# Performance work log

Measured on AMD Instinct MI355X. Metric: run time of the kernel, lower is better.

Reference implementation:

```python
import jax, jax.numpy as jnp
import numpy as np

N_NODES = 50000
N_EDGES = 800000
DIM_IN = 128
DIM_H = 128
DIM_OUT = 10
N_GRAPHS = 256


def _glorot(key, shape):
    lim = float(np.sqrt(6.0 / (shape[0] + shape[1])))
    return jax.random.uniform(key, shape, jnp.float32, -lim, lim)


def setup_inputs() -> dict:
    key = jax.random.key(0)
    ks = jax.random.split(key, 8)
    x = jax.random.normal(ks[0], (N_NODES, DIM_IN), jnp.float32)
    edge_index = jax.random.randint(ks[1], (2, N_EDGES), 0, N_NODES, dtype=jnp.int64)
    batch = jnp.sort(jax.random.randint(ks[2], (N_NODES,), 0, N_GRAPHS, dtype=jnp.int64))
    return {
        'x': x,
        'edge_index': edge_index,
        'batch': batch,
        'W1': _glorot(ks[3], (DIM_IN, DIM_H)),
        'b1': jnp.zeros((DIM_H,), jnp.float32),
        'W2': _glorot(ks[4], (DIM_H, DIM_H)),
        'b2': jnp.zeros((DIM_H,), jnp.float32),
        'Wl1': _glorot(ks[5], (2 * DIM_H, 2 * DIM_H)),
        'bl1': jnp.zeros((2 * DIM_H,), jnp.float32),
        'Wl2': _glorot(ks[6], (2 * DIM_H, DIM_OUT)),
        'bl2': jnp.zeros((DIM_OUT,), jnp.float32),
    }


def _gcn_conv(h, W, b, src, dst, norm, n):
    # x @ W, gather source rows, scale by symmetric norm, scatter-add to dest
    m = (h @ W)[src] * norm[:, None]          # [E+N, dim_h]
    return jax.ops.segment_sum(m, dst, num_segments=n) + b


def reference(x, edge_index, batch, W1, b1, W2, b2, Wl1, bl1, Wl2, bl2):
    n = x.shape[0]
    loops = jnp.arange(n, dtype=edge_index.dtype)
    src = jnp.concatenate([edge_index[0], loops])  # add self-loops (PyG GCNConv default)
    dst = jnp.concatenate([edge_index[1], loops])
    deg = jax.ops.segment_sum(jnp.ones_like(dst, x.dtype), dst, num_segments=n)
    dinv = jnp.where(deg > 0, jax.lax.rsqrt(jnp.maximum(deg, 1.0)), 0.0)
    norm = dinv[src] * dinv[dst]
    # eval mode: dropout is identity
    h1 = _gcn_conv(x, W1, b1, src, dst, norm, n)
    h2 = _gcn_conv(h1, W2, b2, src, dst, norm, n)
    g1 = jax.ops.segment_sum(h1, batch, num_segments=N_GRAPHS)  # global_add_pool
    g2 = jax.ops.segment_sum(h2, batch, num_segments=N_GRAPHS)
    g = jnp.concatenate([g1, g2], axis=1)  # [N_GRAPHS, 2*dim_h]
    h = jax.nn.relu(g @ Wl1 + bl1)
    h = h @ Wl2 + bl2
    return (h, jax.nn.log_softmax(h, axis=1))
```

## Files before the change

### kernel.cpp

```cpp
#include <hip/hip_runtime.h>
#include <hip/hip_bf16.h>
#include <math.h>


#define DIMH 128
#define EBCAP 8192
#define SCAT_CHUNK 2048

typedef __attribute__((ext_vector_type(8))) short s16x8;
typedef __attribute__((ext_vector_type(4))) float f32x4;

__device__ inline ushort f2b(float f) {
    uint u = __float_as_uint(f);
    return (ushort)((u + 0x7fffu + ((u >> 16) & 1u)) >> 16);
}
__device__ inline uint pack2(float lo, float hi) {
    return (uint)f2b(lo) | ((uint)f2b(hi) << 16);
}
__device__ inline float blo(uint u) { return __uint_as_float(u << 16); }
__device__ inline float bhi(uint u) { return __uint_as_float(u & 0xffff0000u); }

__global__ __launch_bounds__(256) void k_front(const int* __restrict__ src,
                                               const int* __restrict__ dst,
                                               int* __restrict__ bcnt,
                                               uint* __restrict__ ebuf, int E, int scnb,
                                               const float* __restrict__ x,
                                               ushort* __restrict__ Xb, int n8, int cvnb,
                                               const float* __restrict__ W1,
                                               const float* __restrict__ W2,
                                               ushort* __restrict__ WT1,
                                               ushort* __restrict__ WT2) {
    __shared__ int h[4][256];
    __shared__ int wb[4][256];
    int blk = blockIdx.x;
    int t = threadIdx.x;
    if (blk < scnb) {
        int wave = t >> 6;
        h[0][t] = 0; h[1][t] = 0; h[2][t] = 0; h[3][t] = 0;
        __syncthreads();
        int e0 = blk * SCAT_CHUNK;
        int e1 = e0 + SCAT_CHUNK; if (e1 > E) e1 = E;
        for (int e = e0 + t; e < e1; e += 256)
            atomicAdd(&h[wave][dst[e] >> 8], 1);
        __syncthreads();
        {
            int h0 = h[0][t], h1 = h[1][t], h2 = h[2][t], h3 = h[3][t];
            int tot = h0 + h1 + h2 + h3;
            int gb = tot ? atomicAdd(&bcnt[t], tot) : 0;
            wb[0][t] = gb;
            wb[1][t] = gb + h0;
            wb[2][t] = gb + h0 + h1;
            wb[3][t] = gb + h0 + h1 + h2;
            h[0][t] = 0; h[1][t] = 0; h[2][t] = 0; h[3][t] = 0;
        }
        __syncthreads();
        for (int e = e0 + t; e < e1; e += 256) {
            int d = dst[e];
            int bk = d >> 8;
            int rank = wb[wave][bk] + atomicAdd(&h[wave][bk], 1);
            if (rank < EBCAP)
                ebuf[(size_t)bk * EBCAP + rank] = ((uint)(d & 255) << 24) | (uint)src[e];
        }
    } else if (blk < scnb + cvnb) {
        int i = (blk - scnb) * 256 + t;
        if (i < n8) {
            const float4* in4 = (const float4*)x;
            float4 a = in4[2 * i], b = in4[2 * i + 1];
            uint4 o;
            o.x = pack2(a.x, a.y); o.y = pack2(a.z, a.w);
            o.z = pack2(b.x, b.y); o.w = pack2(b.z, b.w);
            *(uint4*)(Xb + (size_t)i * 8) = o;
        }
    } else {
        int idx = (blk - scnb - cvnb) * 256 + t;
        const float* W = (idx < 16384) ? W1 : W2;
        ushort* WT = (idx < 16384) ? WT1 : WT2;
        int tt = idx & 16383;
        int k = tt >> 7, nn = tt & 127;
        WT[nn * 128 + k] = f2b(W[tt]);
    }
}

__global__ __launch_bounds__(256) void k_bcsr(const uint* __restrict__ ebuf,
                                              const int* __restrict__ bcnt,
                                              float* __restrict__ dinv,
                                              int2* __restrict__ rng,
                                              int* __restrict__ srt, int n) {
    __shared__ int cnt[256];
    __shared__ int wsum[4];
    __shared__ int stage[EBCAP];
    int b = blockIdx.x;
    int t = threadIdx.x;
    int c = bcnt[b]; if (c > EBCAP) c = EBCAP;
    size_t B = (size_t)b * EBCAP;
    cnt[t] = 0;
    __syncthreads();
    for (int i = t; i < c; i += 256)
        atomicAdd(&cnt[ebuf[B + i] >> 24], 1);
    __syncthreads();
    int v = cnt[t];
    int incl = v;
    for (int k = 1; k < 64; k <<= 1) {
        int u = __shfl_up(incl, k, 64);
        if ((t & 63) >= k) incl += u;
    }
    if ((t & 63) == 63) wsum[t >> 6] = incl;
    __syncthreads();
    int add = 0;
    for (int j = 0; j < (t >> 6); ++j) add += wsum[j];
    incl += add;
    int loc = incl - v;
    int node = b * 256 + t;
    if (node < n) {
        dinv[node] = rsqrtf((float)(v + 1));
        rng[node] = make_int2((int)B + loc, (int)B + loc + v);
    }
    cnt[t] = loc;
    __syncthreads();
    for (int i = t; i < c; i += 256) {
        uint r = ebuf[B + i];
        int p = atomicAdd(&cnt[r >> 24], 1);
        stage[p] = (int)(r & 0xffffffu);
    }
    __syncthreads();
    for (int i = t; i < c; i += 256) srt[B + i] = stage[i];
}

__device__ __forceinline__ void gemm_body(const ushort* __restrict__ Xb,
                                          const ushort* __restrict__ WT,
                                          const float* __restrict__ scale,
                                          ushort* __restrict__ P, int n,
                                          int blk, ushort* lds) {
    ushort* Xs = lds;
    ushort* Ws = lds + 64 * 128;
    const int tid = threadIdx.x;
    const int row0 = blk * 64;
    for (int ci = tid; ci < 1024; ci += 256) {
        int r = ci >> 4, c16 = ci & 15;
        uint dstB = (uint)(r * 256 + c16 * 16) ^ (uint)((r & 7) << 4);
        uint4 v = make_uint4(0u, 0u, 0u, 0u);
        if (row0 + r < n) v = *(const uint4*)(Xb + (size_t)(row0 + r) * 128 + c16 * 8);
        *(uint4*)((char*)Xs + dstB) = v;
    }
    for (int ci = tid; ci < 2048; ci += 256) {
        int r = ci >> 4, c16 = ci & 15;
        uint dstB = (uint)(r * 256 + c16 * 16) ^ (uint)((r & 7) << 4);
        *(uint4*)((char*)Ws + dstB) = *(const uint4*)(WT + (size_t)r * 128 + c16 * 8);
    }
    __syncthreads();
    const int wave = tid >> 6, lane = tid & 63;
    const int l15 = lane & 15, g = lane >> 4;
    f32x4 acc[8];
#pragma unroll
    for (int nt = 0; nt < 8; ++nt) acc[nt] = (f32x4){0.f, 0.f, 0.f, 0.f};
    const int tr = wave * 16 + l15;
    const uint aswz = (uint)((tr & 7) << 4);
#pragma unroll
    for (int kk = 0; kk < 4; ++kk) {
        uint aB = ((uint)(tr * 256 + kk * 64 + g * 16)) ^ aswz;
        s16x8 afrag = *(const s16x8*)((const char*)Xs + aB);
#pragma unroll
        for (int nt = 0; nt < 8; ++nt) {
            int wr = nt * 16 + l15;
            uint bB = ((uint)(wr * 256 + kk * 64 + g * 16)) ^ ((uint)((wr & 7) << 4));
            s16x8 bfrag = *(const s16x8*)((const char*)Ws + bB);
            acc[nt] = __builtin_amdgcn_mfma_f32_16x16x32_bf16(afrag, bfrag, acc[nt], 0, 0, 0);
        }
    }
    float sc[4];
#pragma unroll
    for (int reg = 0; reg < 4; ++reg) {
        int grow = row0 + wave * 16 + g * 4 + reg;
        sc[reg] = (grow < n) ? scale[grow] : 0.f;
    }
#pragma unroll
    for (int nt = 0; nt < 8; ++nt) {
        int gcol = nt * 16 + l15;
#pragma unroll
        for (int reg = 0; reg < 4; ++reg) {
            int grow = row0 + wave * 16 + g * 4 + reg;
            if (grow < n) P[(size_t)grow * 128 + gcol] = f2b(sc[reg] * acc[nt][reg]);
        }
    }
}

__global__ __launch_bounds__(256) void k_gemm(const ushort* __restrict__ Xb,
                                              const ushort* __restrict__ WT,
                                              const float* __restrict__ scale,
                                              ushort* __restrict__ P, int n) {
    __shared__ ushort lds[64 * 128 + 128 * 128];
    gemm_body(Xb, WT, scale, P, n, blockIdx.x, lds);
}

__device__ __forceinline__ void pool_body(const ushort* __restrict__ Hb,
                                          const int* __restrict__ batch,
                                          float* __restrict__ Gpart, int n,
                                          int blk, int* range, float* part) {
    int g = blk >> 2, q = blk & 3;
    if (threadIdx.x < 2) {
        int target = g + threadIdx.x;
        int lo = 0, hi = n;
        while (lo < hi) { int m = (lo + hi) >> 1; if (batch[m] < target) lo = m + 1; else hi = m; }
        range[threadIdx.x] = lo;
    }
    __syncthreads();
    int c = threadIdx.x & 127, h = threadIdx.x >> 7;
    int r = range[0] + q * 2 + h, r1 = range[1];
    float s0 = 0.f, s1 = 0.f;
    for (; r + 8 < r1; r += 16) {
        s0 += __uint_as_float((uint)Hb[(size_t)r       * 128 + c] << 16);
        s1 += __uint_as_float((uint)Hb[(size_t)(r + 8) * 128 + c] << 16);
    }
    for (; r < r1; r += 8) s0 += __uint_as_float((uint)Hb[(size_t)r * 128 + c] << 16);
    part[threadIdx.x] = s0 + s1;
    __syncthreads();
    if (threadIdx.x < 128)
        Gpart[(size_t)blk * 128 + threadIdx.x] = part[threadIdx.x] + part[threadIdx.x + 128];
}

__global__ __launch_bounds__(256) void k_pool(const ushort* __restrict__ Hb,
                                              const int* __restrict__ batch,
                                              float* __restrict__ Gpart, int n) {
    __shared__ int range[2];
    __shared__ float part[256];
    pool_body(Hb, batch, Gpart, n, blockIdx.x, range, part);
}

__global__ __launch_bounds__(256) void k_mid(const ushort* __restrict__ Hb,
                                             const ushort* __restrict__ WT,
                                             const float* __restrict__ scale,
                                             ushort* __restrict__ P, int n, int gemnb,
                                             const int* __restrict__ batch,
                                             float* __restrict__ Gpart) {
    __shared__ ushort lds[64 * 128 + 128 * 128];
    __shared__ int range[2];
    __shared__ float part[256];
    int blk = blockIdx.x;
    if (blk < gemnb) {
        gemm_body(Hb, WT, scale, P, n, blk, lds);
    } else {
        pool_body(Hb, batch, Gpart, n, blk - gemnb, range, part);
    }
}

__global__ __launch_bounds__(256) void k_aggregate(const ushort* __restrict__ Pb,
                                                   const int2* __restrict__ rng,
                                                   const int* __restrict__ srt,
                                                   const float* __restrict__ dinv,
                                                   const float* __restrict__ bias,
                                                   ushort* __restrict__ Hb, int n) {
    int wave = threadIdx.x >> 6;
    int lane = threadIdx.x & 63;
    int i = blockIdx.x * 4 + wave;
    if (i >= n) return;
    int q   = lane >> 4;
    int sub = lane & 15;
    const uint4* P4 = (const uint4*)Pb;
    float a0 = 0.f, a1 = 0.f, a2 = 0.f, a3 = 0.f;
    float a4 = 0.f, a5 = 0.f, a6 = 0.f, a7 = 0.f;
    if (q == 0) {
        uint4 u = P4[(size_t)i * 16 + sub];
        a0 = blo(u.x); a1 = bhi(u.x); a2 = blo(u.y); a3 = bhi(u.y);
        a4 = blo(u.z); a5 = bhi(u.z); a6 = blo(u.w); a7 = bhi(u.w);
    }
    int2 r2 = rng[i];
    int e1 = r2.y;
    int e  = r2.x + q;
    while (e + 12 < e1) {
        int s0 = srt[e], s1 = srt[e + 4], s2 = srt[e + 8], s3 = srt[e + 12];
        uint4 u0 = P4[(size_t)s0 * 16 + sub];
        uint4 u1 = P4[(size_t)s1 * 16 + sub];
        uint4 u2 = P4[(size_t)s2 * 16 + sub];
        uint4 u3 = P4[(size_t)s3 * 16 + sub];
        a0 += (blo(u0.x) + blo(u1.x)) + (blo(u2.x) + blo(u3.x));
        a1 += (bhi(u0.x) + bhi(u1.x)) + (bhi(u2.x) + bhi(u3.x));
        a2 += (blo(u0.y) + blo(u1.y)) + (blo(u2.y) + blo(u3.y));
        a3 += (bhi(u0.y) + bhi(u1.y)) + (bhi(u2.y) + bhi(u3.y));
        a4 += (blo(u0.z) + blo(u1.z)) + (blo(u2.z) + blo(u3.z));
        a5 += (bhi(u0.z) + bhi(u1.z)) + (bhi(u2.z) + bhi(u3.z));
        a6 += (blo(u0.w) + blo(u1.w)) + (blo(u2.w) + blo(u3.w));
        a7 += (bhi(u0.w) + bhi(u1.w)) + (bhi(u2.w) + bhi(u3.w));
        e += 16;
    }
    while (e < e1) {
        uint4 u = P4[(size_t)srt[e] * 16 + sub];
        a0 += blo(u.x); a1 += bhi(u.x); a2 += blo(u.y); a3 += bhi(u.y);
        a4 += blo(u.z); a5 += bhi(u.z); a6 += blo(u.w); a7 += bhi(u.w);
        e += 4;
    }
    a0 += __shfl_xor(a0, 16, 64); a0 += __shfl_xor(a0, 32, 64);
    a1 += __shfl_xor(a1, 16, 64); a1 += __shfl_xor(a1, 32, 64);
    a2 += __shfl_xor(a2, 16, 64); a2 += __shfl_xor(a2, 32, 64);
    a3 += __shfl_xor(a3, 16, 64); a3 += __shfl_xor(a3, 32, 64);
    a4 += __shfl_xor(a4, 16, 64); a4 += __shfl_xor(a4, 32, 64);
    a5 += __shfl_xor(a5, 16, 64); a5 += __shfl_xor(a5, 32, 64);
    a6 += __shfl_xor(a6, 16, 64); a6 += __shfl_xor(a6, 32, 64);
    a7 += __shfl_xor(a7, 16, 64); a7 += __shfl_xor(a7, 32, 64);
    if (q == 0) {
        float di = dinv[i];
        int c = sub * 8;
        float4 b0 = *(const float4*)(bias + c);
        float4 b1 = *(const float4*)(bias + c + 4);
        uint4 o;
        o.x = pack2(fmaf(di, a0, b0.x), fmaf(di, a1, b0.y));
        o.y = pack2(fmaf(di, a2, b0.z), fmaf(di, a3, b0.w));
        o.z = pack2(fmaf(di, a4, b1.x), fmaf(di, a5, b1.y));
        o.w = pack2(fmaf(di, a6, b1.z), fmaf(di, a7, b1.w));
        *(uint4*)(Hb + (size_t)i * 128 + c) = o;
    }
}

__global__ __launch_bounds__(256) void k_mlp(const float* __restrict__ Gp1,
                                             const float* __restrict__ Gp2,
                                             const float* __restrict__ Wl1,
                                             const float* __restrict__ bl1,
                                             const float* __restrict__ Wl2,
                                             const float* __restrict__ bl2,
                                             float* __restrict__ out) {
    __shared__ float gs[256];
    __shared__ float zs[256];
    __shared__ float l[10];
    int g = blockIdx.x, j = threadIdx.x;
    {
        const float* Gp = (j < 128) ? Gp1 : Gp2;
        const float* p = Gp + (size_t)g * 512 + (j & 127);
        gs[j] = (p[0] + p[128]) + (p[256] + p[384]);
    }
    __syncthreads();
    float acc = bl1[j];
    for (int k = 0; k < 256; ++k) acc = fmaf(gs[k], Wl1[k * 256 + j], acc);
    zs[j] = fmaxf(acc, 0.f);
    __syncthreads();
    if (j < 10) {
        float a = bl2[j];
        for (int k = 0; k < 256; ++k) a = fmaf(zs[k], Wl2[k * 10 + j], a);
        l[j] = a;
    }
    __syncthreads();
    if (j < 10) {
        float m = l[0];
        for (int i = 1; i < 10; ++i) m = fmaxf(m, l[i]);
        float s = 0.f;
        for (int i = 0; i < 10; ++i) s += expf(l[i] - m);
        float lse = m + logf(s);
        out[g * 10 + j] = l[j];
        out[2560 + g * 10 + j] = l[j] - lse;
    }
}

static inline size_t alignup(size_t v) { return (v + 255) & ~(size_t)255; }

extern "C" void kernel_launch(void* const* d_in, const int* in_sizes, int n_in,
                              void* d_out, int out_size, void* d_ws, size_t ws_size,
                              hipStream_t stream) {
    const float* x    = (const float*)d_in[0];
    const int*   edge = (const int*)d_in[1];
    const int*   batch= (const int*)d_in[2];
    const float* W1   = (const float*)d_in[3];
    const float* b1   = (const float*)d_in[4];
    const float* W2   = (const float*)d_in[5];
    const float* b2   = (const float*)d_in[6];
    const float* Wl1  = (const float*)d_in[7];
    const float* bl1  = (const float*)d_in[8];
    const float* Wl2  = (const float*)d_in[9];
    const float* bl2  = (const float*)d_in[10];

    const int N = in_sizes[2];
    const int E = in_sizes[1] / 2;
    const int* srcIdx = edge;
    const int* dstIdx = edge + E;

    const int nb = (N + 255) >> 8;

    char* ws = (char*)d_ws;
    ushort* Xb    = (ushort*)ws; ws += alignup((size_t)N * DIMH * 2);
    ushort* P     = (ushort*)ws; ws += alignup((size_t)N * DIMH * 2);
    ushort* Hb    = (ushort*)ws; ws += alignup((size_t)N * DIMH * 2);
    ushort* WT1   = (ushort*)ws; ws += alignup((size_t)128 * 128 * 2);
    ushort* WT2   = (ushort*)ws; ws += alignup((size_t)128 * 128 * 2);
    float*  dinv  = (float*)ws;  ws += alignup((size_t)N * 4);
    int2*   rng   = (int2*)ws;   ws += alignup((size_t)N * 8);
    int*    srt   = (int*)ws;    ws += alignup((size_t)nb * EBCAP * 4);
    uint*   ebuf  = (uint*)ws;   ws += alignup((size_t)nb * EBCAP * 4);
    int*    bcnt  = (int*)ws;    ws += alignup((size_t)256 * 4);
    float*  Gp1   = (float*)ws;  ws += alignup((size_t)1024 * 128 * 4);
    float*  Gp2   = (float*)ws;  ws += alignup((size_t)1024 * 128 * 4);

    const int scnb  = (E + SCAT_CHUNK - 1) / SCAT_CHUNK;
    const int n8    = N * DIMH / 8;
    const int cvnb  = (n8 + 255) / 256;
    const int gemnb = (N + 63) / 64;
    const int aggnb = (N + 3) / 4;

    hipMemsetAsync(bcnt, 0, (size_t)256 * 4, stream);
    k_front<<<scnb + cvnb + 128, 256, 0, stream>>>(srcIdx, dstIdx, bcnt, ebuf, E, scnb,
                                                   x, Xb, n8, cvnb, W1, W2, WT1, WT2);
    k_bcsr<<<nb, 256, 0, stream>>>(ebuf, bcnt, dinv, rng, srt, N);
    k_gemm<<<gemnb, 256, 0, stream>>>(Xb, WT1, dinv, P, N);
    k_aggregate<<<aggnb, 256, 0, stream>>>(P, rng, srt, dinv, b1, Hb, N);
    k_mid<<<gemnb + 1024, 256, 0, stream>>>(Hb, WT2, dinv, P, N, gemnb, batch, Gp1);
    k_aggregate<<<aggnb, 256, 0, stream>>>(P, rng, srt, dinv, b2, Hb, N);
    k_pool<<<1024, 256, 0, stream>>>(Hb, batch, Gp2, N);
    k_mlp<<<256, 256, 0, stream>>>(Gp1, Gp2, Wl1, bl1, Wl2, bl2, (float*)d_out);
}
```

Baseline: 180.9 us.

## Compute degrees in front pass, fuse CSR build with GEMM1 and pool into MLP

The front pass now accumulates per-node in-degree with global atomics, so the layer-1 GEMM no longer waits for the CSR build. That lets the GEMM and CSR-build blocks run in one launch. The final pooling kernel is folded into the MLP kernel, where each graph block sums its own node range, and dinv is recomputed from deg where needed. The change removes two kernel launches and their serialization, at the cost of extra global atomics, a smaller scatter chunk, and a pooled sum done by only 256 blocks.

```diff
diff --git a/kernel.cpp b/kernel.cpp
--- a/kernel.cpp
+++ b/kernel.cpp
@@ -5,7 +5,7 @@
 
 #define DIMH 128
 #define EBCAP 8192
-#define SCAT_CHUNK 2048
+#define SCAT_CHUNK 1024
 
 typedef __attribute__((ext_vector_type(8))) short s16x8;
 typedef __attribute__((ext_vector_type(4))) float f32x4;
@@ -23,6 +23,7 @@
 __global__ __launch_bounds__(256) void k_front(const int* __restrict__ src,
                                                const int* __restrict__ dst,
                                                int* __restrict__ bcnt,
+                                               int* __restrict__ deg,
                                                uint* __restrict__ ebuf, int E, int scnb,
                                                const float* __restrict__ x,
                                                ushort* __restrict__ Xb, int n8, int cvnb,
@@ -40,8 +41,11 @@
         __syncthreads();
         int e0 = blk * SCAT_CHUNK;
         int e1 = e0 + SCAT_CHUNK; if (e1 > E) e1 = E;
-        for (int e = e0 + t; e < e1; e += 256)
-            atomicAdd(&h[wave][dst[e] >> 8], 1);
+        for (int e = e0 + t; e < e1; e += 256) {
+            int d = dst[e];
+            atomicAdd(&h[wave][d >> 8], 1);
+            atomicAdd(&deg[d], 1);
+        }
         __syncthreads();
         {
             int h0 = h[0][t], h1 = h[1][t], h2 = h[2][t], h3 = h[3][t];
@@ -81,15 +85,11 @@
     }
 }
 
-__global__ __launch_bounds__(256) void k_bcsr(const uint* __restrict__ ebuf,
-                                              const int* __restrict__ bcnt,
-                                              float* __restrict__ dinv,
-                                              int2* __restrict__ rng,
-                                              int* __restrict__ srt, int n) {
-    __shared__ int cnt[256];
-    __shared__ int wsum[4];
-    __shared__ int stage[EBCAP];
-    int b = blockIdx.x;
+__device__ __forceinline__ void bcsr_body(const uint* __restrict__ ebuf,
+                                          const int* __restrict__ bcnt,
+                                          int2* __restrict__ rng,
+                                          int* __restrict__ srt, int n,
+                                          int b, int* cnt, int* wsum, int* stage) {
     int t = threadIdx.x;
     int c = bcnt[b]; if (c > EBCAP) c = EBCAP;
     size_t B = (size_t)b * EBCAP;
@@ -111,10 +111,7 @@
     incl += add;
     int loc = incl - v;
     int node = b * 256 + t;
-    if (node < n) {
-        dinv[node] = rsqrtf((float)(v + 1));
-        rng[node] = make_int2((int)B + loc, (int)B + loc + v);
-    }
+    if (node < n) rng[node] = make_int2((int)B + loc, (int)B + loc + v);
     cnt[t] = loc;
     __syncthreads();
     for (int i = t; i < c; i += 256) {
@@ -128,7 +125,7 @@
 
 __device__ __forceinline__ void gemm_body(const ushort* __restrict__ Xb,
                                           const ushort* __restrict__ WT,
-                                          const float* __restrict__ scale,
+                                          const int* __restrict__ deg,
                                           ushort* __restrict__ P, int n,
                                           int blk, ushort* lds) {
     ushort* Xs = lds;
@@ -171,7 +168,7 @@
 #pragma unroll
     for (int reg = 0; reg < 4; ++reg) {
         int grow = row0 + wave * 16 + g * 4 + reg;
-        sc[reg] = (grow < n) ? scale[grow] : 0.f;
+        sc[reg] = (grow < n) ? rsqrtf((float)(deg[grow] + 1)) : 0.f;
     }
 #pragma unroll
     for (int nt = 0; nt < 8; ++nt) {
@@ -184,12 +181,24 @@
     }
 }
 
-__global__ __launch_bounds__(256) void k_gemm(const ushort* __restrict__ Xb,
-                                              const ushort* __restrict__ WT,
-                                              const float* __restrict__ scale,
-                                              ushort* __restrict__ P, int n) {
+__global__ __launch_bounds__(256) void k_g1csr(const ushort* __restrict__ Xb,
+                                               const ushort* __restrict__ WT1,
+                                               const int* __restrict__ deg,
+                                               ushort* __restrict__ P, int n, int gemnb,
+                                               const uint* __restrict__ ebuf,
+                                               const int* __restrict__ bcnt,
+                                               int2* __restrict__ rng,
+                                               int* __restrict__ srt) {
     __shared__ ushort lds[64 * 128 + 128 * 128];
-    gemm_body(Xb, WT, scale, P, n, blockIdx.x, lds);
+    int blk = blockIdx.x;
+    if (blk < gemnb) {
+        gemm_body(Xb, WT1, deg, P, n, blk, lds);
+    } else {
+        int* cnt   = (int*)lds;
+        int* wsum  = cnt + 256;
+        int* stage = wsum + 8;
+        bcsr_body(ebuf, bcnt, rng, srt, n, blk - gemnb, cnt, wsum, stage);
+    }
 }
 
 __device__ __forceinline__ void pool_body(const ushort* __restrict__ Hb,
@@ -218,17 +227,9 @@
         Gpart[(size_t)blk * 128 + threadIdx.x] = part[threadIdx.x] + part[threadIdx.x + 128];
 }
 
-__global__ __launch_bounds__(256) void k_pool(const ushort* __restrict__ Hb,
-                                              const int* __restrict__ batch,
-                                              float* __restrict__ Gpart, int n) {
-    __shared__ int range[2];
-    __shared__ float part[256];
-    pool_body(Hb, batch, Gpart, n, blockIdx.x, range, part);
-}
-
 __global__ __launch_bounds__(256) void k_mid(const ushort* __restrict__ Hb,
                                              const ushort* __restrict__ WT,
-                                             const float* __restrict__ scale,
+                                             const int* __restrict__ deg,
                                              ushort* __restrict__ P, int n, int gemnb,
                                              const int* __restrict__ batch,
                                              float* __restrict__ Gpart) {
@@ -237,7 +238,7 @@
     __shared__ float part[256];
     int blk = blockIdx.x;
     if (blk < gemnb) {
-        gemm_body(Hb, WT, scale, P, n, blk, lds);
+        gemm_body(Hb, WT, deg, P, n, blk, lds);
     } else {
         pool_body(Hb, batch, Gpart, n, blk - gemnb, range, part);
     }
@@ -246,7 +247,7 @@
 __global__ __launch_bounds__(256) void k_aggregate(const ushort* __restrict__ Pb,
                                                    const int2* __restrict__ rng,
                                                    const int* __restrict__ srt,
-                                                   const float* __restrict__ dinv,
+                                                   const int* __restrict__ deg,
                                                    const float* __restrict__ bias,
                                                    ushort* __restrict__ Hb, int n) {
     int wave = threadIdx.x >> 6;
@@ -297,7 +298,7 @@
     a6 += __shfl_xor(a6, 16, 64); a6 += __shfl_xor(a6, 32, 64);
     a7 += __shfl_xor(a7, 16, 64); a7 += __shfl_xor(a7, 32, 64);
     if (q == 0) {
-        float di = dinv[i];
+        float di = rsqrtf((float)(deg[i] + 1));
         int c = sub * 8;
         float4 b0 = *(const float4*)(bias + c);
         float4 b1 = *(const float4*)(bias + c + 4);
@@ -311,7 +312,8 @@
 }
 
 __global__ __launch_bounds__(256) void k_mlp(const float* __restrict__ Gp1,
-                                             const float* __restrict__ Gp2,
+                                             const ushort* __restrict__ Hb,
+                                             const int* __restrict__ batch, int n,
                                              const float* __restrict__ Wl1,
                                              const float* __restrict__ bl1,
                                              const float* __restrict__ Wl2,
@@ -319,12 +321,35 @@
                                              float* __restrict__ out) {
     __shared__ float gs[256];
     __shared__ float zs[256];
+    __shared__ float part[256];
     __shared__ float l[10];
+    __shared__ int range[2];
     int g = blockIdx.x, j = threadIdx.x;
+    if (j < 2) {
+        int target = g + j;
+        int lo = 0, hi = n;
+        while (lo < hi) { int m = (lo + hi) >> 1; if (batch[m] < target) lo = m + 1; else hi = m; }
+        range[j] = lo;
+    }
+    __syncthreads();
     {
-        const float* Gp = (j < 128) ? Gp1 : Gp2;
-        const float* p = Gp + (size_t)g * 512 + (j & 127);
+        int c = j & 127, h = j >> 7;
+        int r = range[0] + h, r1 = range[1];
+        float s0 = 0.f, s1 = 0.f, s2 = 0.f, s3 = 0.f;
+        for (; r + 6 < r1; r += 8) {
+            s0 += __uint_as_float((uint)Hb[(size_t)r       * 128 + c] << 16);
+            s1 += __uint_as_float((uint)Hb[(size_t)(r + 2) * 128 + c] << 16);
+            s2 += __uint_as_float((uint)Hb[(size_t)(r + 4) * 128 + c] << 16);
+            s3 += __uint_as_float((uint)Hb[(size_t)(r + 6) * 128 + c] << 16);
+        }
+        for (; r < r1; r += 2) s0 += __uint_as_float((uint)Hb[(size_t)r * 128 + c] << 16);
+        part[j] = (s0 + s1) + (s2 + s3);
+    }
+    __syncthreads();
+    if (j < 128) {
+        const float* p = Gp1 + (size_t)g * 512 + j;
         gs[j] = (p[0] + p[128]) + (p[256] + p[384]);
+        gs[128 + j] = part[j] + part[j + 128];
     }
     __syncthreads();
     float acc = bl1[j];
@@ -378,13 +403,12 @@
     ushort* Hb    = (ushort*)ws; ws += alignup((size_t)N * DIMH * 2);
     ushort* WT1   = (ushort*)ws; ws += alignup((size_t)128 * 128 * 2);
     ushort* WT2   = (ushort*)ws; ws += alignup((size_t)128 * 128 * 2);
-    float*  dinv  = (float*)ws;  ws += alignup((size_t)N * 4);
+    int*    bcnt  = (int*)ws;    ws += alignup((size_t)256 * 4);
+    int*    deg   = (int*)ws;    ws += alignup((size_t)N * 4);
     int2*   rng   = (int2*)ws;   ws += alignup((size_t)N * 8);
     int*    srt   = (int*)ws;    ws += alignup((size_t)nb * EBCAP * 4);
     uint*   ebuf  = (uint*)ws;   ws += alignup((size_t)nb * EBCAP * 4);
-    int*    bcnt  = (int*)ws;    ws += alignup((size_t)256 * 4);
     float*  Gp1   = (float*)ws;  ws += alignup((size_t)1024 * 128 * 4);
-    float*  Gp2   = (float*)ws;  ws += alignup((size_t)1024 * 128 * 4);
 
     const int scnb  = (E + SCAT_CHUNK - 1) / SCAT_CHUNK;
     const int n8    = N * DIMH / 8;
@@ -392,14 +416,13 @@
     const int gemnb = (N + 63) / 64;
     const int aggnb = (N + 3) / 4;
 
-    hipMemsetAsync(bcnt, 0, (size_t)256 * 4, stream);
-    k_front<<<scnb + cvnb + 128, 256, 0, stream>>>(srcIdx, dstIdx, bcnt, ebuf, E, scnb,
+    hipMemsetAsync(bcnt, 0, alignup((size_t)256 * 4) + (size_t)N * 4, stream);
+    k_front<<<scnb + cvnb + 128, 256, 0, stream>>>(srcIdx, dstIdx, bcnt, deg, ebuf, E, scnb,
                                                    x, Xb, n8, cvnb, W1, W2, WT1, WT2);
-    k_bcsr<<<nb, 256, 0, stream>>>(ebuf, bcnt, dinv, rng, srt, N);
-    k_gemm<<<gemnb, 256, 0, stream>>>(Xb, WT1, dinv, P, N);
-    k_aggregate<<<aggnb, 256, 0, stream>>>(P, rng, srt, dinv, b1, Hb, N);
-    k_mid<<<gemnb + 1024, 256, 0, stream>>>(Hb, WT2, dinv, P, N, gemnb, batch, Gp1);
-    k_aggregate<<<aggnb, 256, 0, stream>>>(P, rng, srt, dinv, b2, Hb, N);
-    k_pool<<<1024, 256, 0, stream>>>(Hb, batch, Gp2, N);
-    k_mlp<<<256, 256, 0, stream>>>(Gp1, Gp2, Wl1, bl1, Wl2, bl2, (float*)d_out);
-}
+    k_g1csr<<<gemnb + nb, 256, 0, stream>>>(Xb, WT1, deg, P, N, gemnb,
+                                            ebuf, bcnt, rng, srt);
+    k_aggregate<<<aggnb, 256, 0, stream>>>(P, rng, srt, deg, b1, Hb, N);
+    k_mid<<<gemnb + 1024, 256, 0, stream>>>(Hb, WT2, deg, P, N, gemnb, batch, Gp1);
+    k_aggregate<<<aggnb, 256, 0, stream>>>(P, rng, srt, deg, b2, Hb, N);
+    k_mlp<<<256, 256, 0, stream>>>(Gp1, Hb, batch, N, Wl1, bl1, Wl2, bl2, (float*)d_out);
+}
```

Result: slower. 203.2 us (+12.3%).
